# Kernel optimization log

Hardware: AMD Instinct MI355X
Metric: run time of the kernel (lower is better)

## Reference

```python
import jax, jax.numpy as jnp
import numpy as np
from jax import lax

B, C, N = 4, 512, 4096
NH = 8
HD = C // NH          # 64
SR = 2                # sr_ratio
EPS = 1e-5            # BatchNorm eps (torch default)


def setup_inputs() -> dict:
    key = jax.random.key(0)
    ks = jax.random.split(key, 12)
    d = {}
    d["x"] = jax.random.normal(ks[0], (B, C, N), jnp.float32)
    d["y"] = jax.random.normal(ks[1], (B, C, N), jnp.float32)  # unused by forward (faithful to source)
    # Conv1d kernel-size-1 weights == (out_c, in_c) matrices; trunc_normal std=0.02 ~ normal*0.02
    d["Wq"] = jax.random.normal(ks[2], (C, C), jnp.float32) * 0.02
    d["Wk"] = jax.random.normal(ks[3], (C, C), jnp.float32) * 0.02
    # sr: Conv2d(dim, dim, kernel=SR, stride=SR), kaiming-ish init per _init_weights
    fan_out = SR * SR * C
    d["Wsr"] = jax.random.normal(ks[4], (C, C, SR, SR), jnp.float32) * np.sqrt(2.0 / fan_out)
    d["bsr"] = jnp.zeros((C,), jnp.float32)
    # BatchNorm1d(dim) in inference mode
    d["bn_gamma"] = 1.0 + 0.1 * jax.random.normal(ks[5], (C,), jnp.float32)
    d["bn_beta"] = 0.1 * jax.random.normal(ks[6], (C,), jnp.float32)
    d["bn_mean"] = 0.1 * jax.random.normal(ks[7], (C,), jnp.float32)
    d["bn_var"] = 1.0 + 0.1 * jnp.abs(jax.random.normal(ks[8], (C,), jnp.float32))
    d["Wproj"] = jax.random.normal(ks[9], (C, C), jnp.float32) * 0.02
    d["bproj"] = jnp.zeros((C,), jnp.float32)
    d["H"] = 64
    d["W"] = 64
    return d


def reference(x, y, Wq, Wk, Wsr, bsr, bn_gamma, bn_beta, bn_mean, bn_var, Wproj, bproj, H, W):
    scale = HD ** -0.5
    # q: Conv1d(k=1) -> (B,C,N) -> (B,NH,HD,N) -> (B,NH,N,HD)
    q = jnp.einsum('oc,bcn->bon', Wq, x).reshape(B, NH, HD, N).transpose(0, 1, 3, 2)
    # spatial reduction path (sr_ratio > 1): Conv2d stride SR, then BN (inference), then k-proj
    x4 = x.reshape(B, C, H, W)
    xsr = lax.conv_general_dilated(x4, Wsr, (SR, SR), 'VALID',
                                   dimension_numbers=('NCHW', 'OIHW', 'NCHW'))
    xsr = xsr + bsr[None, :, None, None]
    xsr = xsr.reshape(B, C, -1)  # (B, C, Nk), Nk = (H//SR)*(W//SR)
    inv_std = lax.rsqrt(bn_var + EPS)
    xsr = (xsr - bn_mean[None, :, None]) * (inv_std * bn_gamma)[None, :, None] + bn_beta[None, :, None]
    k = jnp.einsum('oc,bcn->bon', Wk, xsr).reshape(B, NH, HD, -1)  # (B,NH,HD,Nk)
    # v: mean over tokens, replicated per head -> effectively (B, C)
    v = jnp.mean(x, axis=2)  # (B, C)
    # scores + max over keys (no softmax)
    attn = jnp.einsum('bhnd,bhdk->bhnk', q, k) * scale  # (B,NH,N,Nk)
    attn = jnp.max(attn, axis=-1)                        # (B,NH,N)
    # out[b,c,n] = sum_h attn[b,h,n] * v[b,c]  (attn^T @ v, then transpose)
    out = jnp.sum(attn, axis=1)[:, None, :] * v[:, :, None]  # (B,C,N)
    out = jnp.einsum('oc,bcn->bon', Wproj, out) + bproj[None, :, None]
    return out
```

## Files before the change

kernel.cpp:

```cpp
#include <hip/hip_runtime.h>
#include <hip/hip_bf16.h>

constexpr int B_ = 4, C_ = 512, N_ = 4096, NH_ = 8, HD_ = 64;
constexpr int NK = 1024;
constexpr float SCALE = 0.125f;
constexpr float EPS = 1e-5f;

typedef __attribute__((ext_vector_type(8))) short bf16x8;
typedef __attribute__((ext_vector_type(4))) float f32x4;

__device__ __forceinline__ short bf16s(float f) {
    __hip_bfloat16 h = __float2bfloat16(f);
    return *reinterpret_cast<short*>(&h);
}
__device__ __forceinline__ float bf2f(short s) {
    return __bfloat162float(*reinterpret_cast<__hip_bfloat16*>(&s));
}

#define GLD16(gp, lp)                                                                     \
    __builtin_amdgcn_global_load_lds((const __attribute__((address_space(1))) void*)(gp), \
                                     (__attribute__((address_space(3))) void*)(lp), 16, 0, 0)

__global__ __launch_bounds__(256) void k_xw(const float* __restrict__ x,
                                            const float* __restrict__ Wq, const float* __restrict__ Wk,
                                            const float* __restrict__ gamma, const float* __restrict__ beta,
                                            const float* __restrict__ mean, const float* __restrict__ var,
                                            const float* __restrict__ bsr, const float* __restrict__ Wsr,
                                            short* __restrict__ xT, float* __restrict__ vpart,
                                            short* __restrict__ Wq16, short* __restrict__ Wkp16,
                                            float* __restrict__ bk, short* __restrict__ WsrT) {
    const int bid = blockIdx.x, tid = threadIdx.x;
    __shared__ float t[64][65];
    if (bid < 2048) {
        const int y = bid & 63, ct = (bid >> 6) & 7, b = bid >> 9;
        {
            const int cc = tid >> 2, q = tid & 3;
            const float* xr = x + ((size_t)(b * C_ + ct * 64 + cc)) * N_ + y * 64;
            float s = 0.f;
#pragma unroll
            for (int jj = 0; jj < 4; ++jj) {
                float4 f = *reinterpret_cast<const float4*>(&xr[q * 16 + jj * 4]);
                int n = q * 16 + jj * 4;
                t[n + 0][cc] = f.x; t[n + 1][cc] = f.y;
                t[n + 2][cc] = f.z; t[n + 3][cc] = f.w;
                s += f.x + f.y + f.z + f.w;
            }
            s += __shfl_xor(s, 1);
            s += __shfl_xor(s, 2);
            if (q == 0) vpart[((size_t)(y * B_ + b)) * C_ + ct * 64 + cc] = s;
        }
        __syncthreads();
        {
            const int n = tid >> 2, c0 = (tid & 3) * 16;
            bf16x8 u0, u1;
#pragma unroll
            for (int j = 0; j < 8; ++j) {
                u0[j] = bf16s(t[n][c0 + j]);
                u1[j] = bf16s(t[n][c0 + 8 + j]);
            }
            short* dst = xT + ((size_t)(b * N_ + y * 64 + n)) * C_ + ct * 64 + c0;
            *reinterpret_cast<bf16x8*>(dst) = u0;
            *reinterpret_cast<bf16x8*>(dst + 8) = u1;
        }
    } else if (bid < 2560) {
        const int o = bid - 2048;
        float acc = 0.f;
        for (int c = tid; c < C_; c += 256) {
            float sc = rsqrtf(var[c] + EPS) * gamma[c];
            float wk = Wk[o * C_ + c];
            Wkp16[o * C_ + c] = bf16s(wk * sc);
            Wq16[o * C_ + c] = bf16s(Wq[o * C_ + c]);
            acc += wk * (sc * (bsr[c] - mean[c]) + beta[c]);
        }
        for (int m = 32; m; m >>= 1) acc += __shfl_xor(acc, m);
        if ((tid & 63) == 0) t[0][tid >> 6] = acc;
        __syncthreads();
        if (tid == 0) bk[o] = t[0][0] + t[0][1] + t[0][2] + t[0][3];
    } else {
        const int r = bid - 2560, kt = r & 31, ot = r >> 5;
        {
            const int cc = tid >> 2, q = tid & 3;
            const float* xr = Wsr + (size_t)(ot * 64 + cc) * 2048 + kt * 64;
#pragma unroll
            for (int jj = 0; jj < 4; ++jj) {
                float4 f = *reinterpret_cast<const float4*>(&xr[q * 16 + jj * 4]);
                int n = q * 16 + jj * 4;
                t[n + 0][cc] = f.x; t[n + 1][cc] = f.y;
                t[n + 2][cc] = f.z; t[n + 3][cc] = f.w;
            }
        }
        __syncthreads();
        {
            const int n = tid >> 2, c0 = (tid & 3) * 16;
            bf16x8 u0, u1;
#pragma unroll
            for (int j = 0; j < 8; ++j) {
                u0[j] = bf16s(t[n][c0 + j]);
                u1[j] = bf16s(t[n][c0 + 8 + j]);
            }
            int gkk = kt * 64 + n;
            int row2 = (gkk & 3) * 512 + (gkk >> 2);
            short* dst = WsrT + (size_t)row2 * C_ + ot * 64 + c0;
            *reinterpret_cast<bf16x8*>(dst) = u0;
            *reinterpret_cast<bf16x8*>(dst + 8) = u1;
        }
    }
}

template <int MT>
__device__ __forceinline__ void gemm_core(const short* __restrict__ Ag,
                                          const short* __restrict__ Bg, int K,
                                          short* Abuf, short* Bbuf,
                                          f32x4 (&acc)[MT][4]) {
    const int tid = threadIdx.x;
    const int w = tid >> 6, l = tid & 63;
    const int lr = l & 15, lg = l >> 4;
    const int wm = w >> 1, wn = w & 1;
    const int srow = tid >> 3, scol = (tid & 7) * 8;
    char* AbufC = (char*)Abuf;
    char* BbufC = (char*)Bbuf;
    for (int kt = 0; kt < K; kt += 64) {
#pragma unroll
        for (int i = 0; i < MT; ++i)
            GLD16(Ag + (size_t)(i * 32 + srow) * K + kt + scol, AbufC + i * 4096 + tid * 16);
#pragma unroll
        for (int i = 0; i < 4; ++i)
            GLD16(Bg + (size_t)(i * 32 + srow) * K + kt + scol, BbufC + i * 4096 + tid * 16);
        __syncthreads();
        bf16x8 af[MT][2], bfv[4][2];
#pragma unroll
        for (int mt = 0; mt < MT; ++mt)
#pragma unroll
            for (int ks = 0; ks < 2; ++ks)
                af[mt][ks] = *reinterpret_cast<const bf16x8*>(
                    &Abuf[(wm * MT * 16 + mt * 16 + lr) * 64 + ks * 32 + lg * 8]);
#pragma unroll
        for (int nt = 0; nt < 4; ++nt)
#pragma unroll
            for (int ks = 0; ks < 2; ++ks)
                bfv[nt][ks] = *reinterpret_cast<const bf16x8*>(
                    &Bbuf[(wn * 64 + nt * 16 + lr) * 64 + ks * 32 + lg * 8]);
#pragma unroll
        for (int mt = 0; mt < MT; ++mt)
#pragma unroll
            for (int nt = 0; nt < 4; ++nt) {
                acc[mt][nt] = __builtin_amdgcn_mfma_f32_16x16x32_bf16(af[mt][0], bfv[nt][0], acc[mt][nt], 0, 0, 0);
                acc[mt][nt] = __builtin_amdgcn_mfma_f32_16x16x32_bf16(af[mt][1], bfv[nt][1], acc[mt][nt], 0, 0, 0);
            }
        __syncthreads();
    }
}

__global__ __launch_bounds__(256) void k_wckpv(const short* __restrict__ WsrT,
                                               const short* __restrict__ Wkp16,
                                               const float* __restrict__ vpart,
                                               const float* __restrict__ Wproj,
                                               short* __restrict__ Wck16,
                                               float* __restrict__ pv) {
    const int bid = blockIdx.x, tid = threadIdx.x;
    if (bid < 256) {
        __shared__ short Ab[64 * 64];
        __shared__ short Bb[64 * 64];
        const int m0 = (bid & 31) * 64;
        const int n0 = (bid >> 5) * 64;
        const int w = tid >> 6, l = tid & 63;
        const int lr = l & 15, lg = l >> 4, wm = w >> 1, wn = w & 1;
        const int srow = tid >> 3, scol = (tid & 7) * 8;
        f32x4 acc[2][2];
#pragma unroll
        for (int i = 0; i < 2; ++i)
#pragma unroll
            for (int j = 0; j < 2; ++j) acc[i][j] = (f32x4){0.f, 0.f, 0.f, 0.f};
        char* AbC = (char*)Ab;
        char* BbC = (char*)Bb;
        for (int kt = 0; kt < 512; kt += 64) {
#pragma unroll
            for (int j = 0; j < 2; ++j) {
                GLD16(WsrT + (size_t)(m0 + j * 32 + srow) * 512 + kt + scol, AbC + j * 4096 + tid * 16);
                GLD16(Wkp16 + (size_t)(n0 + j * 32 + srow) * 512 + kt + scol, BbC + j * 4096 + tid * 16);
            }
            __syncthreads();
            bf16x8 af[2][2], bfv[2][2];
#pragma unroll
            for (int mt = 0; mt < 2; ++mt)
#pragma unroll
                for (int ks = 0; ks < 2; ++ks)
                    af[mt][ks] = *reinterpret_cast<const bf16x8*>(
                        &Ab[(wm * 32 + mt * 16 + lr) * 64 + ks * 32 + lg * 8]);
#pragma unroll
            for (int nt = 0; nt < 2; ++nt)
#pragma unroll
                for (int ks = 0; ks < 2; ++ks)
                    bfv[nt][ks] = *reinterpret_cast<const bf16x8*>(
                        &Bb[(wn * 32 + nt * 16 + lr) * 64 + ks * 32 + lg * 8]);
#pragma unroll
            for (int mt = 0; mt < 2; ++mt)
#pragma unroll
                for (int nt = 0; nt < 2; ++nt) {
                    acc[mt][nt] = __builtin_amdgcn_mfma_f32_16x16x32_bf16(af[mt][0], bfv[nt][0], acc[mt][nt], 0, 0, 0);
                    acc[mt][nt] = __builtin_amdgcn_mfma_f32_16x16x32_bf16(af[mt][1], bfv[nt][1], acc[mt][nt], 0, 0, 0);
                }
            __syncthreads();
        }
#pragma unroll
        for (int mt = 0; mt < 2; ++mt)
#pragma unroll
            for (int nt = 0; nt < 2; ++nt) {
                int kk0 = m0 + wm * 32 + mt * 16 + lg * 4;
                int o = n0 + wn * 32 + nt * 16 + lr;
                short4 u;
                u.x = bf16s(acc[mt][nt][0]);
                u.y = bf16s(acc[mt][nt][1]);
                u.z = bf16s(acc[mt][nt][2]);
                u.w = bf16s(acc[mt][nt][3]);
                *reinterpret_cast<short4*>(&Wck16[(size_t)o * 2048 + kk0]) = u;
            }
    } else {
        const int r = bid - 256, oc = r & 7, b = r >> 3;
        __shared__ float vs[512];
        float2 s = {0.f, 0.f};
        for (int y = 0; y < 64; ++y) {
            float2 f = *reinterpret_cast<const float2*>(&vpart[((size_t)(y * B_ + b)) * C_ + tid * 2]);
            s.x += f.x; s.y += f.y;
        }
        vs[tid * 2] = s.x * (1.f / N_);
        vs[tid * 2 + 1] = s.y * (1.f / N_);
        __syncthreads();
        const int w = tid >> 6, l = tid & 63;
#pragma unroll 4
        for (int i = 0; i < 16; ++i) {
            int o = oc * 64 + i * 4 + w;
            const float* wr = Wproj + (size_t)o * C_;
            float4 a = *reinterpret_cast<const float4*>(&wr[l * 8]);
            float4 b4 = *reinterpret_cast<const float4*>(&wr[l * 8 + 4]);
            float acc = a.x * vs[l * 8] + a.y * vs[l * 8 + 1] + a.z * vs[l * 8 + 2] + a.w * vs[l * 8 + 3] +
                        b4.x * vs[l * 8 + 4] + b4.y * vs[l * 8 + 5] + b4.z * vs[l * 8 + 6] + b4.w * vs[l * 8 + 7];
            for (int m = 32; m; m >>= 1) acc += __shfl_xor(acc, m);
            if (l == 0) pv[b * C_ + o] = acc;
        }
    }
}

__global__ __launch_bounds__(256) void k_gemm_qk2(const short* __restrict__ xT,
                                                  const short* __restrict__ Wq16,
                                                  const short* __restrict__ Wck16,
                                                  short* __restrict__ kp,
                                                  short* __restrict__ q2) {
    __shared__ short Abuf[128 * 64];
    __shared__ short Bbuf[128 * 64];
    f32x4 acc[4][4];
#pragma unroll
    for (int i = 0; i < 4; ++i)
#pragma unroll
        for (int j = 0; j < 4; ++j) acc[i][j] = (f32x4){0.f, 0.f, 0.f, 0.f};
    const int bid = (blockIdx.x & 7) * 128 + (blockIdx.x >> 3);
    const int tid = threadIdx.x, l = tid & 63, w = tid >> 6;
    const int lr = l & 15, lg = l >> 4, wm = w >> 1, wn = w & 1;
    const int srow = tid >> 3, scol = (tid & 7) * 8;
    char* AbufC = (char*)Abuf;
    char* BbufC = (char*)Bbuf;

    if (bid < 512) {
        const int s = bid >> 7;
        const int dy = s >> 1, dx = s & 1;
        const int r2 = bid & 127;
        const int n0 = (r2 >> 2) * 128;
        const int m0 = (r2 & 3) * 128;
        for (int kt2 = 0; kt2 < 512; kt2 += 64) {
#pragma unroll
            for (int i = 0; i < 4; ++i) {
                int bp = n0 + i * 32 + srow;
                int b = bp >> 10, p = bp & 1023;
                int n = ((p >> 5) * 2 + dy) * 64 + (p & 31) * 2 + dx;
                GLD16(xT + ((size_t)(b * N_ + n)) * C_ + kt2 + scol, AbufC + i * 4096 + tid * 16);
            }
#pragma unroll
            for (int i = 0; i < 4; ++i)
                GLD16(Wck16 + (size_t)(m0 + i * 32 + srow) * 2048 + s * 512 + kt2 + scol,
                      BbufC + i * 4096 + tid * 16);
            __syncthreads();
            bf16x8 af[4][2], bfv[4][2];
#pragma unroll
            for (int mt = 0; mt < 4; ++mt)
#pragma unroll
                for (int ks = 0; ks < 2; ++ks)
                    af[mt][ks] = *reinterpret_cast<const bf16x8*>(
                        &Abuf[(wm * 64 + mt * 16 + lr) * 64 + ks * 32 + lg * 8]);
#pragma unroll
            for (int nt = 0; nt < 4; ++nt)
#pragma unroll
                for (int ks = 0; ks < 2; ++ks)
                    bfv[nt][ks] = *reinterpret_cast<const bf16x8*>(
                        &Bbuf[(wn * 64 + nt * 16 + lr) * 64 + ks * 32 + lg * 8]);
#pragma unroll
            for (int mt = 0; mt < 4; ++mt)
#pragma unroll
                for (int nt = 0; nt < 4; ++nt) {
                    acc[mt][nt] = __builtin_amdgcn_mfma_f32_16x16x32_bf16(af[mt][0], bfv[nt][0], acc[mt][nt], 0, 0, 0);
                    acc[mt][nt] = __builtin_amdgcn_mfma_f32_16x16x32_bf16(af[mt][1], bfv[nt][1], acc[mt][nt], 0, 0, 0);
                }
            __syncthreads();
        }
        short* kps = kp + (size_t)s * (4096 * 512);
#pragma unroll
        for (int mt = 0; mt < 4; ++mt)
#pragma unroll
            for (int nt = 0; nt < 4; ++nt) {
                int o = m0 + wn * 64 + nt * 16 + lr;
#pragma unroll
                for (int r = 0; r < 4; ++r) {
                    int bp = n0 + wm * 64 + mt * 16 + lg * 4 + r;
                    kps[(size_t)bp * 512 + o] = bf16s(acc[mt][nt][r]);
                }
            }
    } else {
        const int bq = bid - 512;
        const int m0 = (bq & 3) * 128, n0 = (bq >> 2) * 128;
        gemm_core<4>(Wq16 + (size_t)m0 * 512, xT + (size_t)n0 * 512, 512, Abuf, Bbuf, acc);
#pragma unroll
        for (int mt = 0; mt < 4; ++mt) {
            const int o0 = m0 + wm * 64 + mt * 16 + lg * 4;
            const int h = o0 >> 6, d0 = o0 & 63;
#pragma unroll
            for (int nt = 0; nt < 4; ++nt) {
                int ng = n0 + wn * 64 + nt * 16 + lr;
                int b = ng >> 12, n = ng & 4095;
                short4 u;
                u.x = bf16s(acc[mt][nt][0]);
                u.y = bf16s(acc[mt][nt][1]);
                u.z = bf16s(acc[mt][nt][2]);
                u.w = bf16s(acc[mt][nt][3]);
                *reinterpret_cast<short4*>(&q2[(((size_t)(b * NH_ + h)) * N_ + n) * HD_ + d0]) = u;
            }
        }
    }
}

__global__ __launch_bounds__(256) void k_kred(const short* __restrict__ kp,
                                              const float* __restrict__ bk,
                                              short* __restrict__ k3) {
    const int r = blockIdx.x * 4 + (threadIdx.x >> 6);
    const int o0 = (threadIdx.x & 63) * 8;
    const int b = r >> 10, p = r & 1023;
    const short* base = kp + (size_t)r * 512 + o0;
    float s[8];
    float4 b0 = *reinterpret_cast<const float4*>(&bk[o0]);
    float4 b1 = *reinterpret_cast<const float4*>(&bk[o0 + 4]);
    s[0] = b0.x; s[1] = b0.y; s[2] = b0.z; s[3] = b0.w;
    s[4] = b1.x; s[5] = b1.y; s[6] = b1.z; s[7] = b1.w;
#pragma unroll
    for (int sp = 0; sp < 4; ++sp) {
        bf16x8 v = *reinterpret_cast<const bf16x8*>(base + (size_t)sp * (4096 * 512));
#pragma unroll
        for (int j = 0; j < 8; ++j) s[j] += bf2f(v[j]);
    }
    bf16x8 u;
#pragma unroll
    for (int j = 0; j < 8; ++j) u[j] = bf16s(s[j]);
    const int h = o0 >> 6, d = o0 & 63;
    *reinterpret_cast<bf16x8*>(&k3[(((size_t)(b * NH_ + h)) * NK + p) * HD_ + d]) = u;
}

__global__ __launch_bounds__(256) void k_attn3(const short* __restrict__ k3,
                                               const short* __restrict__ q2,
                                               float* __restrict__ am) {
    const int b = blockIdx.z, h = blockIdx.y, n0 = blockIdx.x * 256;
    const int w = threadIdx.x >> 6, l = threadIdx.x & 63;
    const int lr = l & 15, lg = l >> 4;
    const short* qb = q2 + ((size_t)(b * NH_ + h)) * N_ * HD_;
    const short* kb = k3 + ((size_t)(b * NH_ + h)) * NK * HD_;

    bf16x8 bq[16][2];
#pragma unroll
    for (int nt = 0; nt < 16; ++nt)
#pragma unroll
        for (int ks = 0; ks < 2; ++ks)
            bq[nt][ks] = *reinterpret_cast<const bf16x8*>(
                &qb[(size_t)(n0 + nt * 16 + lr) * HD_ + ks * 32 + lg * 8]);

    float rmax[16];
#pragma unroll
    for (int nt = 0; nt < 16; ++nt) rmax[nt] = -3.4e38f;

    const short* kw = kb + (size_t)(w * 256) * HD_;
    const short* s0 = kw + (size_t)lr * HD_ + lg * 8;
    bf16x8 a0 = *reinterpret_cast<const bf16x8*>(s0);
    bf16x8 a1 = *reinterpret_cast<const bf16x8*>(s0 + 32);
    for (int t = 0; t < 16; ++t) {
        bf16x8 c0 = a0, c1 = a1;
        if (t < 15) {
            const short* s2 = kw + (size_t)((t + 1) * 16 + lr) * HD_ + lg * 8;
            a0 = *reinterpret_cast<const bf16x8*>(s2);
            a1 = *reinterpret_cast<const bf16x8*>(s2 + 32);
        }
        __builtin_amdgcn_s_setprio(1);
#pragma unroll
        for (int nt = 0; nt < 16; ++nt) {
            f32x4 acc = {0.f, 0.f, 0.f, 0.f};
            acc = __builtin_amdgcn_mfma_f32_16x16x32_bf16(c0, bq[nt][0], acc, 0, 0, 0);
            acc = __builtin_amdgcn_mfma_f32_16x16x32_bf16(c1, bq[nt][1], acc, 0, 0, 0);
            rmax[nt] = fmaxf(fmaxf(fmaxf(fmaxf(acc[0], acc[1]), acc[2]), acc[3]), rmax[nt]);
        }
        __builtin_amdgcn_s_setprio(0);
    }
#pragma unroll
    for (int nt = 0; nt < 16; ++nt) {
        float m = rmax[nt];
        m = fmaxf(m, __shfl_xor(m, 16));
        m = fmaxf(m, __shfl_xor(m, 32));
        rmax[nt] = m;
    }
    __shared__ float sm[4][256];
    if (lg == 0) {
#pragma unroll
        for (int nt = 0; nt < 16; ++nt) sm[w][nt * 16 + lr] = rmax[nt];
    }
    __syncthreads();
    {
        const int tid = threadIdx.x;
        float m = fmaxf(fmaxf(sm[0][tid], sm[1][tid]),
                        fmaxf(sm[2][tid], sm[3][tid]));
        am[((size_t)(b * NH_ + h)) * N_ + n0 + tid] = SCALE * m;
    }
}

__global__ __launch_bounds__(256) void k_final(const float* __restrict__ pv, const float* __restrict__ am,
                                               const float* __restrict__ bproj, float* __restrict__ out) {
    const int b = blockIdx.z, o0 = blockIdx.y * 64 + (threadIdx.x >> 5) * 8;
    const int n = blockIdx.x * 128 + (threadIdx.x & 31) * 4;
    float4 s = {0.f, 0.f, 0.f, 0.f};
#pragma unroll
    for (int h = 0; h < NH_; ++h) {
        float4 a = *reinterpret_cast<const float4*>(&am[((size_t)(b * NH_ + h)) * N_ + n]);
        s.x += a.x; s.y += a.y; s.z += a.z; s.w += a.w;
    }
    float* ob = out + (size_t)b * C_ * N_ + n;
    const float* pvb = pv + b * C_;
#pragma unroll
    for (int i = 0; i < 8; ++i) {
        int o = o0 + i;
        float p = pvb[o], bp = bproj[o];
        float4 r = {p * s.x + bp, p * s.y + bp, p * s.z + bp, p * s.w + bp};
        *reinterpret_cast<float4*>(&ob[(size_t)o * N_]) = r;
    }
}

extern "C" void kernel_launch(void* const* d_in, const int* in_sizes, int n_in,
                              void* d_out, int out_size, void* d_ws, size_t ws_size,
                              hipStream_t stream) {
    const float* x     = (const float*)d_in[0];
    const float* Wq    = (const float*)d_in[2];
    const float* Wk    = (const float*)d_in[3];
    const float* Wsr   = (const float*)d_in[4];
    const float* bsr   = (const float*)d_in[5];
    const float* gamma = (const float*)d_in[6];
    const float* beta  = (const float*)d_in[7];
    const float* mean  = (const float*)d_in[8];
    const float* var   = (const float*)d_in[9];
    const float* Wproj = (const float*)d_in[10];
    const float* bproj = (const float*)d_in[11];
    float* out = (float*)d_out;

    char* ws = (char*)d_ws;
    float* vpart = (float*)(ws + 0);
    float* pv    = (float*)(ws + 524288);
    float* bk    = (float*)(ws + 532480);
    float* am    = (float*)(ws + 536576);
    short* Wq16  = (short*)(ws + 1060864);
    short* Wkp16 = (short*)(ws + 1585152);
    short* WsrT  = (short*)(ws + 2109440);
    short* Wck16 = (short*)(ws + 4206592);
    short* xT    = (short*)(ws + 6303744);
    short* q2    = (short*)(ws + 23080960);
    short* k3    = (short*)(ws + 39858176);
    short* kp    = (short*)(ws + 44052480);

    k_xw<<<dim3(2816), 256, 0, stream>>>(x, Wq, Wk, gamma, beta, mean, var, bsr, Wsr,
                                         xT, vpart, Wq16, Wkp16, bk, WsrT);
    k_wckpv<<<dim3(288), 256, 0, stream>>>(WsrT, Wkp16, vpart, Wproj, Wck16, pv);
    k_gemm_qk2<<<dim3(1024), 256, 0, stream>>>(xT, Wq16, Wck16, kp, q2);
    k_kred<<<dim3(1024), 256, 0, stream>>>(kp, bk, k3);
    k_attn3<<<dim3(16, NH_, B_), 256, 0, stream>>>(k3, q2, am);
    k_final<<<dim3(32, 8, B_), 256, 0, stream>>>(pv, am, bproj, out);
}
```

Baseline: 92.26 us.

## Fuse split-K reduction of k into GEMM via last-block atomic counter

Removes the separate k_kred kernel. Each of the four spatial-offset GEMM blocks now writes its partial k tile into a tile-local layout and increments a per-tile atomic counter. The last block to finish sums the four partials, adds the bias and writes k3 directly. The counters are zeroed by an extra block in the first kernel. This saves a kernel launch and the global-memory round trip for a separate reduction pass, at the cost of fence/atomic synchronisation and a serial tail in the final block of each tile.

```diff
diff --git a/kernel.cpp b/kernel.cpp
--- a/kernel.cpp
+++ b/kernel.cpp
@@ -28,7 +28,8 @@
                                             const float* __restrict__ bsr, const float* __restrict__ Wsr,
                                             short* __restrict__ xT, float* __restrict__ vpart,
                                             short* __restrict__ Wq16, short* __restrict__ Wkp16,
-                                            float* __restrict__ bk, short* __restrict__ WsrT) {
+                                            float* __restrict__ bk, short* __restrict__ WsrT,
+                                            int* __restrict__ cnt) {
     const int bid = blockIdx.x, tid = threadIdx.x;
     __shared__ float t[64][65];
     if (bid < 2048) {
@@ -76,7 +77,7 @@
         if ((tid & 63) == 0) t[0][tid >> 6] = acc;
         __syncthreads();
         if (tid == 0) bk[o] = t[0][0] + t[0][1] + t[0][2] + t[0][3];
-    } else {
+    } else if (bid < 2816) {
         const int r = bid - 2560, kt = r & 31, ot = r >> 5;
         {
             const int cc = tid >> 2, q = tid & 3;
@@ -104,6 +105,8 @@
             *reinterpret_cast<bf16x8*>(dst) = u0;
             *reinterpret_cast<bf16x8*>(dst + 8) = u1;
         }
+    } else {
+        if (tid < 128) cnt[tid] = 0;
     }
 }
 
@@ -241,11 +244,14 @@
     }
 }
 
-__global__ __launch_bounds__(256) void k_gemm_qk2(const short* __restrict__ xT,
+__global__ __launch_bounds__(256) void k_gemm_qk3(const short* __restrict__ xT,
                                                   const short* __restrict__ Wq16,
                                                   const short* __restrict__ Wck16,
-                                                  short* __restrict__ kp,
-                                                  short* __restrict__ q2) {
+                                                  const float* __restrict__ bk,
+                                                  short* kp,
+                                                  short* __restrict__ q2,
+                                                  short* __restrict__ k3,
+                                                  int* cnt) {
     __shared__ short Abuf[128 * 64];
     __shared__ short Bbuf[128 * 64];
     f32x4 acc[4][4];
@@ -263,9 +269,9 @@
     if (bid < 512) {
         const int s = bid >> 7;
         const int dy = s >> 1, dx = s & 1;
-        const int r2 = bid & 127;
-        const int n0 = (r2 >> 2) * 128;
-        const int m0 = (r2 & 3) * 128;
+        const int tile = bid & 127;
+        const int n0 = (tile >> 2) * 128;
+        const int m0 = (tile & 3) * 128;
         for (int kt2 = 0; kt2 < 512; kt2 += 64) {
 #pragma unroll
             for (int i = 0; i < 4; ++i) {
@@ -301,18 +307,52 @@
                 }
             __syncthreads();
         }
-        short* kps = kp + (size_t)s * (4096 * 512);
+        short* kps = kp + ((size_t)s * 128 + tile) * 16384;
 #pragma unroll
         for (int mt = 0; mt < 4; ++mt)
 #pragma unroll
             for (int nt = 0; nt < 4; ++nt) {
-                int o = m0 + wn * 64 + nt * 16 + lr;
+                int o_local = wn * 64 + nt * 16 + lr;
 #pragma unroll
                 for (int r = 0; r < 4; ++r) {
-                    int bp = n0 + wm * 64 + mt * 16 + lg * 4 + r;
-                    kps[(size_t)bp * 512 + o] = bf16s(acc[mt][nt][r]);
+                    int bp_local = wm * 64 + mt * 16 + lg * 4 + r;
+                    kps[bp_local * 128 + o_local] = bf16s(acc[mt][nt][r]);
                 }
             }
+        __shared__ int sflag;
+        __syncthreads();
+        if (tid == 0) {
+            __threadfence();
+            sflag = (atomicAdd(&cnt[tile], 1) == 3);
+        }
+        __syncthreads();
+        if (sflag) {
+            __threadfence();
+            const int c0 = tid * 64;
+            const int bp = n0 + (c0 >> 7);
+            const int bb = bp >> 10, p = bp & 1023;
+            const int o0 = m0 + (tid & 1) * 64;
+            const int h = o0 >> 6;
+            const size_t tbase = (size_t)tile * 16384 + c0;
+            short* dst = &k3[(((size_t)(bb * NH_ + h)) * NK + p) * HD_];
+#pragma unroll
+            for (int j = 0; j < 8; ++j) {
+                float4 bk0 = *reinterpret_cast<const float4*>(&bk[o0 + j * 8]);
+                float4 bk1 = *reinterpret_cast<const float4*>(&bk[o0 + j * 8 + 4]);
+                float sa[8] = {bk0.x, bk0.y, bk0.z, bk0.w, bk1.x, bk1.y, bk1.z, bk1.w};
+#pragma unroll
+                for (int s2 = 0; s2 < 4; ++s2) {
+                    bf16x8 v = *reinterpret_cast<const bf16x8*>(
+                        &kp[(size_t)s2 * 2097152 + tbase + j * 8]);
+#pragma unroll
+                    for (int jj = 0; jj < 8; ++jj) sa[jj] += bf2f(v[jj]);
+                }
+                bf16x8 u;
+#pragma unroll
+                for (int jj = 0; jj < 8; ++jj) u[jj] = bf16s(sa[jj]);
+                *reinterpret_cast<bf16x8*>(&dst[j * 8]) = u;
+            }
+        }
     } else {
         const int bq = bid - 512;
         const int m0 = (bq & 3) * 128, n0 = (bq >> 2) * 128;
@@ -334,31 +374,6 @@
             }
         }
     }
-}
-
-__global__ __launch_bounds__(256) void k_kred(const short* __restrict__ kp,
-                                              const float* __restrict__ bk,
-                                              short* __restrict__ k3) {
-    const int r = blockIdx.x * 4 + (threadIdx.x >> 6);
-    const int o0 = (threadIdx.x & 63) * 8;
-    const int b = r >> 10, p = r & 1023;
-    const short* base = kp + (size_t)r * 512 + o0;
-    float s[8];
-    float4 b0 = *reinterpret_cast<const float4*>(&bk[o0]);
-    float4 b1 = *reinterpret_cast<const float4*>(&bk[o0 + 4]);
-    s[0] = b0.x; s[1] = b0.y; s[2] = b0.z; s[3] = b0.w;
-    s[4] = b1.x; s[5] = b1.y; s[6] = b1.z; s[7] = b1.w;
-#pragma unroll
-    for (int sp = 0; sp < 4; ++sp) {
-        bf16x8 v = *reinterpret_cast<const bf16x8*>(base + (size_t)sp * (4096 * 512));
-#pragma unroll
-        for (int j = 0; j < 8; ++j) s[j] += bf2f(v[j]);
-    }
-    bf16x8 u;
-#pragma unroll
-    for (int j = 0; j < 8; ++j) u[j] = bf16s(s[j]);
-    const int h = o0 >> 6, d = o0 & 63;
-    *reinterpret_cast<bf16x8*>(&k3[(((size_t)(b * NH_ + h)) * NK + p) * HD_ + d]) = u;
 }
 
 __global__ __launch_bounds__(256) void k_attn3(const short* __restrict__ k3,
@@ -474,12 +489,12 @@
     short* q2    = (short*)(ws + 23080960);
     short* k3    = (short*)(ws + 39858176);
     short* kp    = (short*)(ws + 44052480);
-
-    k_xw<<<dim3(2816), 256, 0, stream>>>(x, Wq, Wk, gamma, beta, mean, var, bsr, Wsr,
-                                         xT, vpart, Wq16, Wkp16, bk, WsrT);
+    int*   cnt   = (int*)(ws + 60829696);
+
+    k_xw<<<dim3(2817), 256, 0, stream>>>(x, Wq, Wk, gamma, beta, mean, var, bsr, Wsr,
+                                         xT, vpart, Wq16, Wkp16, bk, WsrT, cnt);
     k_wckpv<<<dim3(288), 256, 0, stream>>>(WsrT, Wkp16, vpart, Wproj, Wck16, pv);
-    k_gemm_qk2<<<dim3(1024), 256, 0, stream>>>(xT, Wq16, Wck16, kp, q2);
-    k_kred<<<dim3(1024), 256, 0, stream>>>(kp, bk, k3);
+    k_gemm_qk3<<<dim3(1024), 256, 0, stream>>>(xT, Wq16, Wck16, bk, kp, q2, k3, cnt);
     k_attn3<<<dim3(16, NH_, B_), 256, 0, stream>>>(k3, q2, am);
     k_final<<<dim3(32, 8, B_), 256, 0, stream>>>(pv, am, bproj, out);
 }
```

Measured after the change: 261.3 us. 2.83x slower.
